# Performance work log

Hardware: AMD Instinct MI355X
Metric: run time of the kernel (lower is better)

The kernel has to match this reference:

```python
import jax, jax.numpy as jnp
import numpy as np

N_BIT = 8
Q_SCALE = float(1 << N_BIT)        # 256
Q_MAX = (1 << N_BIT) - 1           # 255
MASK = (1 << N_BIT) - 1            # keep only low n_bit bits (carry out of bit 7 dropped)
STRIDE = 1
PADDING = 1


def _quant(x):
    # torch: (x * 2**n_bit).clamp(0, 255).to(int32) -- truncation toward zero; nonneg after clamp
    return jnp.clip(x * Q_SCALE, 0.0, float(Q_MAX)).astype(jnp.int32)


def _im2col(x, k, stride, padding):
    # F.unfold equivalent; patches: [N, C*k*k, h_out, w_out] with channel-major (C, kh, kw) ordering
    patches = jax.lax.conv_general_dilated_patches(
        x, (k, k), (stride, stride), [(padding, padding), (padding, padding)],
        dimension_numbers=("NCHW", "OIHW", "NCHW"))
    N, K, h_out, w_out = patches.shape
    L = h_out * w_out
    # torch: view(N, K, L).permute(1, 2, 0).reshape(K, L*N)
    X_col = patches.reshape(N, K, L).transpose(1, 2, 0).reshape(K, L * N)
    return X_col, h_out, w_out


def _adder_fwd_math(W_col, X_col):
    # mode='logic', table=None => approx full adder is an EXACT full adder over n_bit=8 bits,
    # i.e. (qa + qb) mod 256, then /256, then -sum(|.|) over the K (im2col) axis.
    a = _quant(W_col)[:, :, None]     # [F, K, 1]
    b = _quant(X_col)[None, :, :]     # [1, K, M]
    s = (a + b) & MASK                # [F, K, M] int32
    return -jnp.sum(jnp.abs(s.astype(jnp.float32) / Q_SCALE), axis=1)  # [F, M]


def setup_inputs() -> dict:
    key = jax.random.key(0)
    k1, k2 = jax.random.split(key)
    x = jax.random.normal(k1, (8, 32, 32, 32), dtype=jnp.float32)   # [N, C, H, W]
    W = jax.random.normal(k2, (32, 32, 3, 3), dtype=jnp.float32)    # [F, C, k, k]
    return {"x": x, "W": W}


def reference(x, W):
    F_, C, kh, kw = W.shape
    N = x.shape[0]
    X_col, h_out, w_out = _im2col(x, kh, STRIDE, PADDING)   # [K, L*N]
    W_col = W.reshape(F_, C * kh * kw)                       # [F, K]
    out = _adder_fwd_math(W_col, X_col)                      # [F, L*N]
    out = out.reshape(F_, h_out, w_out, N).transpose(3, 0, 1, 2)  # [N, F, h_out, w_out]
    return out
```

## Files before the change

### kernel.cpp

```cpp
#include <hip/hip_runtime.h>

__device__ __forceinline__ unsigned quantq(float v) {
    v = v * 256.0f;
    v = fminf(fmaxf(v, 0.0f), 255.0f);
    return (unsigned)v;
}

__global__ __launch_bounds__(1024) void adder2d_kernel(
    const float* __restrict__ x, const float* __restrict__ W,
    float* __restrict__ out)
{
    const int tid = threadIdx.x;
    const int bid = blockIdx.x;
    const int n = bid >> 5;
    const int i = bid & 31;

    __shared__ __align__(16) unsigned short sQW[32][296];
    __shared__ __align__(16) unsigned short sQX[32][296];
    __shared__ unsigned char sRow[3072];

    for (int idx = tid; idx < 9216; idx += 1024) {
        int f = idx / 288;
        int k = idx - f * 288;
        sQW[f][k] = (unsigned short)quantq(W[idx]);
    }
    for (int idx = tid; idx < 3072; idx += 1024) {
        int c = idx / 96;
        int rem = idx - c * 96;
        int rr = rem >> 5;
        int w = rem & 31;
        int r = i + rr - 1;
        float v = (r >= 0 && r < 32) ? x[((n * 32 + c) * 32 + r) * 32 + w] : 0.0f;
        sRow[idx] = (unsigned char)quantq(v);
    }
    __syncthreads();

    for (int idx = tid; idx < 9216; idx += 1024) {
        int j = idx / 288;
        int k = idx - j * 288;
        int c = k / 9;
        int rem = k - c * 9;
        int kh = rem / 3;
        int kw = rem - kh * 3;
        int col = j + kw - 1;
        unsigned v = (col >= 0 && col < 32) ? (unsigned)sRow[c * 96 + kh * 32 + col] : 0u;
        sQX[j][k] = (unsigned short)v;
    }
    __syncthreads();

    const int f = tid >> 5;
    const int j = tid & 31;
    const uint4* qwr = (const uint4*)(&sQW[f][0]);
    const uint4* qxr = (const uint4*)(&sQX[j][0]);
    unsigned acc = 0;
#pragma unroll 6
    for (int g = 0; g < 36; ++g) {
        uint4 a = qwr[g];
        uint4 b = qxr[g];
        acc += ((a.x + b.x) & 0x00ff00ffu);
        acc += ((a.y + b.y) & 0x00ff00ffu);
        acc += ((a.z + b.z) & 0x00ff00ffu);
        acc += ((a.w + b.w) & 0x00ff00ffu);
    }
    unsigned total = (acc & 0xffffu) + (acc >> 16);
    out[((n * 32 + f) * 32 + i) * 32 + j] = -(float)total * (1.0f / 256.0f);
}

extern "C" void kernel_launch(void* const* d_in, const int* in_sizes, int n_in,
                              void* d_out, int out_size, void* d_ws, size_t ws_size,
                              hipStream_t stream) {
    const float* x = (const float*)d_in[0];
    const float* W = (const float*)d_in[1];
    float* out = (float*)d_out;
    adder2d_kernel<<<256, 1024, 0, stream>>>(x, W, out);
}
```

Before: 12.85 us.

## Pack 4 quantized bytes per word, use SWAR byte add and v_sad_u8 accumulation

Quantized values are now stored one byte per lane, four to a 32-bit word, instead of as 16-bit halves. Byte-wise mod-256 addition is done with a carry-masking SWAR trick, and v_sad_u8 against zero sums the four bytes into the accumulator. Each thread now computes two output filters and keeps its weight rows in registers, so the block shrinks to 512 threads. The sQX layout is XOR-swizzled to avoid LDS bank conflicts, and global loads use float4. This halves the LDS footprint and per-element ALU work, at the cost of heavy register pressure from 36 uint4 values.

```diff
diff --git a/kernel.cpp b/kernel.cpp
--- a/kernel.cpp
+++ b/kernel.cpp
@@ -1,4 +1,19 @@
 #include <hip/hip_runtime.h>
+
+#define NHB 0x7f7f7f7fu
+#define HIB 0x80808080u
+
+#if __has_builtin(__builtin_amdgcn_sad_u8)
+__device__ __forceinline__ unsigned sad8(unsigned a, unsigned b, unsigned c) {
+    return __builtin_amdgcn_sad_u8(a, b, c);
+}
+#else
+__device__ __forceinline__ unsigned sad8(unsigned a, unsigned b, unsigned c) {
+    unsigned d;
+    asm("v_sad_u8 %0, %1, %2, %3" : "=v"(d) : "v"(a), "v"(b), "v"(c));
+    return d;
+}
+#endif
 
 __device__ __forceinline__ unsigned quantq(float v) {
     v = v * 256.0f;
@@ -6,7 +21,20 @@
     return (unsigned)v;
 }
 
-__global__ __launch_bounds__(1024) void adder2d_kernel(
+__device__ __forceinline__ unsigned pack4(float a, float b, float c, float d) {
+    return quantq(a) | (quantq(b) << 8) | (quantq(c) << 16) | (quantq(d) << 24);
+}
+
+__device__ __forceinline__ void swar2(unsigned a0, unsigned a1, unsigned b,
+                                      unsigned& acc0, unsigned& acc1) {
+    unsigned mb = b & NHB;
+    unsigned s0 = ((a0 & NHB) + mb) ^ ((a0 ^ b) & HIB);
+    unsigned s1 = ((a1 & NHB) + mb) ^ ((a1 ^ b) & HIB);
+    acc0 = sad8(s0, 0u, acc0);
+    acc1 = sad8(s1, 0u, acc1);
+}
+
+__global__ __launch_bounds__(512, 2) void adder2d_kernel(
     const float* __restrict__ x, const float* __restrict__ W,
     float* __restrict__ out)
 {
@@ -15,55 +43,79 @@
     const int n = bid >> 5;
     const int i = bid & 31;
 
-    __shared__ __align__(16) unsigned short sQW[32][296];
-    __shared__ __align__(16) unsigned short sQX[32][296];
-    __shared__ unsigned char sRow[3072];
+    __shared__ unsigned sQW[32 * 72];
+    __shared__ unsigned sQX[32 * 96];
+    __shared__ unsigned sRowW[768];
 
-    for (int idx = tid; idx < 9216; idx += 1024) {
-        int f = idx / 288;
-        int k = idx - f * 288;
-        sQW[f][k] = (unsigned short)quantq(W[idx]);
+    {
+        const float4* W4 = (const float4*)W;
+        for (int m = tid; m < 2304; m += 512) {
+            float4 w = W4[m];
+            sQW[m] = pack4(w.x, w.y, w.z, w.w);
+        }
     }
-    for (int idx = tid; idx < 3072; idx += 1024) {
-        int c = idx / 96;
-        int rem = idx - c * 96;
-        int rr = rem >> 5;
-        int w = rem & 31;
-        int r = i + rr - 1;
-        float v = (r >= 0 && r < 32) ? x[((n * 32 + c) * 32 + r) * 32 + w] : 0.0f;
-        sRow[idx] = (unsigned char)quantq(v);
+    for (int m = tid; m < 768; m += 512) {
+        int c = m / 24;
+        int r = m - c * 24;
+        int kh = r >> 3;
+        int wq = (r & 7) << 2;
+        int row = i + kh - 1;
+        unsigned pv = 0;
+        if (row >= 0 && row < 32) {
+            float4 v = *(const float4*)&x[((n * 32 + c) * 32 + row) * 32 + wq];
+            pv = pack4(v.x, v.y, v.z, v.w);
+        }
+        sRowW[m] = pv;
     }
     __syncthreads();
 
-    for (int idx = tid; idx < 9216; idx += 1024) {
-        int j = idx / 288;
-        int k = idx - j * 288;
-        int c = k / 9;
-        int rem = k - c * 9;
-        int kh = rem / 3;
-        int kw = rem - kh * 3;
-        int col = j + kw - 1;
-        unsigned v = (col >= 0 && col < 32) ? (unsigned)sRow[c * 96 + kh * 32 + col] : 0u;
-        sQX[j][k] = (unsigned short)v;
+    {
+        const unsigned char* sRow = (const unsigned char*)sRowW;
+        for (int m = tid; m < 2304; m += 512) {
+            int j = m / 72;
+            int p = m - j * 72;
+            unsigned v = 0;
+#pragma unroll
+            for (int e = 0; e < 4; ++e) {
+                int k = 4 * p + e;
+                int c = k / 9;
+                int r = k - 9 * c;
+                int kh = r / 3;
+                int kw = r - 3 * kh;
+                int col = j + kw - 1;
+                unsigned bv = (col >= 0 && col < 32) ? (unsigned)sRow[c * 96 + kh * 32 + col] : 0u;
+                v |= bv << (8 * e);
+            }
+            int g = p >> 2, e2 = p & 3;
+            sQX[j * 96 + ((g ^ (j & 7)) << 2) + e2] = v;
+        }
+    }
+
+    const int f = tid >> 5;
+    const int j = tid & 31;
+    uint4 qa[18], qb[18];
+    {
+        const uint4* r0 = (const uint4*)&sQW[f * 72];
+        const uint4* r1 = (const uint4*)&sQW[(f + 16) * 72];
+#pragma unroll
+        for (int g = 0; g < 18; ++g) { qa[g] = r0[g]; qb[g] = r1[g]; }
     }
     __syncthreads();
 
-    const int f = tid >> 5;
-    const int j = tid & 31;
-    const uint4* qwr = (const uint4*)(&sQW[f][0]);
-    const uint4* qxr = (const uint4*)(&sQX[j][0]);
-    unsigned acc = 0;
-#pragma unroll 6
-    for (int g = 0; g < 36; ++g) {
-        uint4 a = qwr[g];
-        uint4 b = qxr[g];
-        acc += ((a.x + b.x) & 0x00ff00ffu);
-        acc += ((a.y + b.y) & 0x00ff00ffu);
-        acc += ((a.z + b.z) & 0x00ff00ffu);
-        acc += ((a.w + b.w) & 0x00ff00ffu);
+    unsigned acc0 = 0, acc1 = 0;
+    const uint4* qx = (const uint4*)&sQX[j * 96];
+    const int js = j & 7;
+#pragma unroll
+    for (int g = 0; g < 18; ++g) {
+        uint4 bv = qx[g ^ js];
+        swar2(qa[g].x, qb[g].x, bv.x, acc0, acc1);
+        swar2(qa[g].y, qb[g].y, bv.y, acc0, acc1);
+        swar2(qa[g].z, qb[g].z, bv.z, acc0, acc1);
+        swar2(qa[g].w, qb[g].w, bv.w, acc0, acc1);
     }
-    unsigned total = (acc & 0xffffu) + (acc >> 16);
-    out[((n * 32 + f) * 32 + i) * 32 + j] = -(float)total * (1.0f / 256.0f);
+
+    out[((n * 32 + f) * 32 + i) * 32 + j]        = -(float)acc0 * (1.0f / 256.0f);
+    out[((n * 32 + f + 16) * 32 + i) * 32 + j]   = -(float)acc1 * (1.0f / 256.0f);
 }
 
 extern "C" void kernel_launch(void* const* d_in, const int* in_sizes, int n_in,
@@ -72,5 +124,5 @@
     const float* x = (const float*)d_in[0];
     const float* W = (const float*)d_in[1];
     float* out = (float*)d_out;
-    adder2d_kernel<<<256, 1024, 0, stream>>>(x, W, out);
+    adder2d_kernel<<<256, 512, 0, stream>>>(x, W, out);
 }
```

Measured after the change: 17.17 us. +33.6%, slower.
